# Kernel optimization log

Measured on AMD Instinct MI355X. Metric: run time of the kernel, lower is better.

Reference implementation:

```python
import jax, jax.numpy as jnp
import numpy as np

HIDDEN = 4096
N_HEADS = 32
N_KV_HEADS = 8
HEAD_DIM = HIDDEN // N_HEADS  # 128
N_REP = N_HEADS // N_KV_HEADS  # 4
ROPE_THETA = 10000.0
B, S = 2, 2048


def setup_inputs() -> dict:
    key = jax.random.key(0)
    ks = jax.random.split(key, 9)
    sc = 1.0 / np.sqrt(HIDDEN)
    query = jax.random.normal(ks[0], (B, S, HIDDEN), jnp.float32)
    key_t = jax.random.normal(ks[1], (B, S, HIDDEN), jnp.float32)
    value = jax.random.normal(ks[2], (B, S, HIDDEN), jnp.float32)
    position_ids = jnp.sort(jax.random.randint(ks[3], (B, S), 0, S), axis=-1)
    Wq = jax.random.normal(ks[4], (HIDDEN, N_HEADS * HEAD_DIM), jnp.float32) * sc
    Wk = jax.random.normal(ks[5], (HIDDEN, N_KV_HEADS * HEAD_DIM), jnp.float32) * sc
    Wv = jax.random.normal(ks[6], (HIDDEN, N_KV_HEADS * HEAD_DIM), jnp.float32) * sc
    Wo = jax.random.normal(ks[7], (N_HEADS * HEAD_DIM, HIDDEN), jnp.float32) * sc
    return {"query": query, "key": key_t, "value": value,
            "position_ids": position_ids,
            "Wq": Wq, "Wk": Wk, "Wv": Wv, "Wo": Wo}


def _rotate_half(x):
    x1, x2 = jnp.split(x, 2, axis=-1)
    return jnp.concatenate((-x2, x1), axis=-1)


def _rope_cos_sin(position_ids):
    # inv_freq: [head_dim/2]
    inv_freq = 1.0 / (ROPE_THETA ** (jnp.arange(0, HEAD_DIM, 2, dtype=jnp.float32) / HEAD_DIM))
    # freqs: [B, S, head_dim/2] via per-position lookup (equiv. to cache gather cos_cached[position_ids])
    freqs = position_ids[..., None].astype(jnp.float32) * inv_freq
    emb = jnp.concatenate((freqs, freqs), axis=-1)          # [B, S, head_dim]
    return jnp.cos(emb)[:, None, :, :], jnp.sin(emb)[:, None, :, :]  # [B,1,S,hd]


def reference(query, key, value, position_ids, Wq, Wk, Wv, Wo):
    nb, q_len, _ = query.shape
    # QKV projections (bias-free linear)
    q = jnp.einsum('bse,ef->bsf', query, Wq).reshape(nb, q_len, N_HEADS, HEAD_DIM).transpose(0, 2, 1, 3)
    k = jnp.einsum('bse,ef->bsf', key, Wk).reshape(nb, q_len, N_KV_HEADS, HEAD_DIM).transpose(0, 2, 1, 3)
    v = jnp.einsum('bse,ef->bsf', value, Wv).reshape(nb, q_len, N_KV_HEADS, HEAD_DIM).transpose(0, 2, 1, 3)
    # RoPE
    cos, sin = _rope_cos_sin(position_ids)
    q = q * cos + _rotate_half(q) * sin
    k = k * cos + _rotate_half(k) * sin
    # GQA repeat_kv: [B, kvH, S, d] -> [B, H, S, d]
    k = jnp.repeat(k, N_REP, axis=1)
    v = jnp.repeat(v, N_REP, axis=1)
    # scaled dot-product attention (flash-attn semantics, no padding mask)
    scale = 1.0 / jnp.sqrt(jnp.asarray(HEAD_DIM, q.dtype))
    scores = jnp.einsum('bhqd,bhkd->bhqk', q, k) * scale
    probs = jax.nn.softmax(scores, axis=-1)
    ctx = jnp.einsum('bhqk,bhkd->bhqd', probs, v)
    ctx = ctx.transpose(0, 2, 1, 3).reshape(nb, q_len, N_HEADS * HEAD_DIM)
    return jnp.einsum('bsf,fe->bse', ctx, Wo)
```

## Files before the change

kernel.cpp:

```cpp
#include <hip/hip_runtime.h>
#include <hip/hip_bf16.h>

typedef __attribute__((ext_vector_type(8))) short bf16x8;
typedef __attribute__((ext_vector_type(4))) float f32x4;
typedef __attribute__((ext_vector_type(16))) float f32x16;
typedef __attribute__((ext_vector_type(2))) unsigned uint2x;

#define AS1(p) ((const __attribute__((address_space(1))) void*)(p))
#define AS3(p) ((__attribute__((address_space(3))) void*)(p))

__device__ inline unsigned cvtpk_bf16(float lo, float hi) {
  unsigned r;
  asm("v_cvt_pk_bf16_f32 %0, %1, %2" : "=v"(r) : "v"(lo), "v"(hi));
  return r;
}

__device__ inline uint2x plswap(unsigned a, unsigned b) {
  return __builtin_amdgcn_permlane32_swap(a, b, false, false);
}


__global__ __launch_bounds__(256) void xconv_kv(const float* __restrict__ k_in,
                                                const float* __restrict__ v_in,
                                                __hip_bfloat16* __restrict__ kc,
                                                __hip_bfloat16* __restrict__ vc) {
  const float* in = blockIdx.y ? v_in : k_in;
  __hip_bfloat16* out = blockIdx.y ? vc : kc;
  size_t i = ((size_t)blockIdx.x * 256 + threadIdx.x) * 4;
  float4 v = *(const float4*)(in + i);
  union { __hip_bfloat16 h[4]; ushort4 u; } o;
  o.h[0] = __float2bfloat16(v.x);
  o.h[1] = __float2bfloat16(v.y);
  o.h[2] = __float2bfloat16(v.z);
  o.h[3] = __float2bfloat16(v.w);
  *(ushort4*)(out + i) = o.u;
}

__global__ __launch_bounds__(256) void xconv(const float* __restrict__ in,
                                             __hip_bfloat16* __restrict__ out) {
  size_t i = ((size_t)blockIdx.x * 256 + threadIdx.x) * 4;
  float4 v = *(const float4*)(in + i);
  union { __hip_bfloat16 h[4]; ushort4 u; } o;
  o.h[0] = __float2bfloat16(v.x);
  o.h[1] = __float2bfloat16(v.y);
  o.h[2] = __float2bfloat16(v.z);
  o.h[3] = __float2bfloat16(v.w);
  *(ushort4*)(out + i) = o.u;
}

__global__ __launch_bounds__(256) void wtransAll(const float* __restrict__ Wq,
                                                 const float* __restrict__ Wo,
                                                 const float* __restrict__ Wk,
                                                 const float* __restrict__ Wv,
                                                 __hip_bfloat16* __restrict__ WqT,
                                                 __hip_bfloat16* __restrict__ WoT,
                                                 __hip_bfloat16* __restrict__ WkT,
                                                 __hip_bfloat16* __restrict__ WvT) {
  const int z = blockIdx.z;
  const int N = (z < 2) ? 4096 : 1024;
  const int n0 = blockIdx.x << 6;
  if (n0 >= N) return;
  const float* W = (z == 0) ? Wq : (z == 1) ? Wo : (z == 2) ? Wk : Wv;
  __hip_bfloat16* WT = (z == 0) ? WqT : (z == 1) ? WoT : (z == 2) ? WkT : WvT;
  __shared__ float t[64][68];
  const int k0 = blockIdx.y << 6;
  const int tx = threadIdx.x & 15, ty = threadIdx.x >> 4;
#pragma unroll
  for (int j = 0; j < 4; ++j) {
    const int k = ty + j * 16;
    float4 v = *(const float4*)(W + (size_t)(k0 + k) * N + n0 + tx * 4);
    t[tx * 4 + 0][k] = v.x;
    t[tx * 4 + 1][k] = v.y;
    t[tx * 4 + 2][k] = v.z;
    t[tx * 4 + 3][k] = v.w;
  }
  __syncthreads();
#pragma unroll
  for (int j = 0; j < 4; ++j) {
    const int n = ty + j * 16;
    float4 v = *(const float4*)(&t[n][tx * 4]);
    union { __hip_bfloat16 h[4]; ushort4 u; } o;
    o.h[0] = __float2bfloat16(v.x);
    o.h[1] = __float2bfloat16(v.y);
    o.h[2] = __float2bfloat16(v.z);
    o.h[3] = __float2bfloat16(v.w);
    *(ushort4*)(WT + (size_t)(n0 + n) * 4096 + k0 + tx * 4) = o.u;
  }
}

__global__ __launch_bounds__(256) void rope(__hip_bfloat16* __restrict__ X,
                                            const int* __restrict__ pos,
                                            int hbits, float scale) {
  const int t = blockIdx.x * 256 + threadIdx.x;
  const int j = t & 63;
  const int rest = t >> 6;
  const int h = rest & ((1 << hbits) - 1);
  const int row = rest >> hbits;
  const float p = (float)pos[row];
  const float fr = p * exp2f((float)j * -0.2076205059304601f);
  float sn, cs;
  __sincosf(fr, &sn, &cs);
  const size_t base = (((size_t)row << hbits) + h) * 128 + j;
  const float x0 = __bfloat162float(X[base]);
  const float x1 = __bfloat162float(X[base + 64]);
  X[base]      = __float2bfloat16((x0 * cs - x1 * sn) * scale);
  X[base + 64] = __float2bfloat16((x1 * cs + x0 * sn) * scale);
}


__device__ inline int tile_off(int row, int k) {
  return (((row >> 4) << 1) + (k >> 5)) * 512 + (row & 15) * 32 +
         ((k & 31) ^ ((row & 8) << 1));
}

__device__ inline void stageA(const __hip_bfloat16* __restrict__ src, int ld, int row0,
                              int kt, int h, __hip_bfloat16* ldsT, int w, int lane) {
#pragma unroll
  for (int li = 0; li < 2; ++li) {
    const int t = li * 8 + w;
    const int grp = ((t >> 3) << 1) + h;
    const int srl = (t & 7) >> 1, sk = t & 1;
    const int rowbase = grp * 64 + srl * 16;
    __hip_bfloat16* dst = ldsT + ((((rowbase >> 4) << 1) + sk) << 9);
    const int r = lane >> 2;
    const int ku = (lane & 3) ^ ((r & 8) >> 2);
    __builtin_amdgcn_global_load_lds(
        AS1(src + (size_t)(row0 + rowbase + r) * ld + kt + (sk << 5) + (ku << 3)),
        AS3(dst), 16, 0, 0);
  }
}

__device__ inline void stageB(const __hip_bfloat16* __restrict__ src, int ld, int col0,
                              int kt, int h, __hip_bfloat16* ldsT, int w, int lane) {
#pragma unroll
  for (int li = 0; li < 2; ++li) {
    const int t = li * 8 + w;
    const int q = t >> 2;
    const int srl = (t >> 1) & 1, sk = t & 1;
    const int colbase = q * 64 + h * 32 + srl * 16;
    __hip_bfloat16* dst = ldsT + ((((colbase >> 4) << 1) + sk) << 9);
    const int r = lane >> 2;
    const int ku = (lane & 3) ^ ((r & 8) >> 2);
    __builtin_amdgcn_global_load_lds(
        AS1(src + (size_t)(col0 + colbase + r) * ld + kt + (sk << 5) + (ku << 3)),
        AS3(dst), 16, 0, 0);
  }
}

template <int OUT_F32>
__global__ __launch_bounds__(512, 1) void gemm256(const __hip_bfloat16* __restrict__ A,
                                                  const __hip_bfloat16* __restrict__ BT,
                                                  void* __restrict__ Cout,
                                                  int M, int N, int K) {
  __shared__ __align__(16) __hip_bfloat16 lds[2][2][16384];
  const int tid = threadIdx.x;
  const int lane = tid & 63, w = tid >> 6;
  const int l15 = lane & 15, lg = lane >> 4;
  const int wm = w >> 2, wn = w & 3;
  const int nbx = N >> 8;
  const int nwg = (M >> 8) * nbx;
  const int bid = blockIdx.x;
  const int swz = (bid & 7) * (nwg >> 3) + (bid >> 3);
  const int m0 = (swz / nbx) << 8, n0 = (swz % nbx) << 8;

  f32x4 acc[8][4] = {};
  const int NT = K >> 6;

  stageA(A, K, m0, 0, 0, &lds[0][0][0], w, lane);
  stageB(BT, K, n0, 0, 0, &lds[0][1][0], w, lane);
  stageA(A, K, m0, 0, 1, &lds[0][0][0], w, lane);
  stageB(BT, K, n0, 0, 1, &lds[0][1][0], w, lane);
  stageA(A, K, m0, 64, 0, &lds[1][0][0], w, lane);
  stageB(BT, K, n0, 64, 0, &lds[1][1][0], w, lane);
  asm volatile("s_waitcnt vmcnt(4)" ::: "memory");
  __builtin_amdgcn_s_barrier();

  for (int j = 0; j < NT; ++j) {
    const int buf = j & 1;
    const __hip_bfloat16* Ab = &lds[buf][0][0];
    const __hip_bfloat16* Bb = &lds[buf][1][0];
    __hip_bfloat16* An = &lds[buf ^ 1][0][0];
    __hip_bfloat16* Bn = &lds[buf ^ 1][1][0];
    __hip_bfloat16* Ac = &lds[buf][0][0];
    __hip_bfloat16* Bc = &lds[buf][1][0];
    const int kt1 = (j + 1) << 6, kt2 = (j + 2) << 6;
    const bool s1 = (j + 1) < NT, s2 = (j + 2) < NT;

    auto phase = [&](int rq, int cq, int sid) {
      bf16x8 af[2][4], bfr[2][2];
#pragma unroll
      for (int kk = 0; kk < 2; ++kk) {
#pragma unroll
        for (int rf = 0; rf < 4; ++rf)
          af[kk][rf] = *(const bf16x8*)(Ab +
              tile_off(wm * 128 + (rq * 4 + rf) * 16 + l15, kk * 32 + lg * 8));
#pragma unroll
        for (int cf = 0; cf < 2; ++cf)
          bfr[kk][cf] = *(const bf16x8*)(Bb +
              tile_off(wn * 64 + (cq * 2 + cf) * 16 + l15, kk * 32 + lg * 8));
      }
      if (sid == 0)      { if (s1) stageA(A, K, m0, kt1, 1, An, w, lane); }
      else if (sid == 1) { if (s1) stageB(BT, K, n0, kt1, 1, Bn, w, lane); }
      else if (sid == 2) { if (s2) stageA(A, K, m0, kt2, 0, Ac, w, lane); }
      else {
        if (s2) stageB(BT, K, n0, kt2, 0, Bc, w, lane);
        if (s2) asm volatile("s_waitcnt vmcnt(4)" ::: "memory");
        else    asm volatile("s_waitcnt vmcnt(0)" ::: "memory");
      }
      __builtin_amdgcn_s_barrier();
      asm volatile("s_waitcnt lgkmcnt(0)" ::: "memory");
      __builtin_amdgcn_sched_barrier(0);
      __builtin_amdgcn_s_setprio(1);
#pragma unroll
      for (int kk = 0; kk < 2; ++kk)
#pragma unroll
        for (int rf = 0; rf < 4; ++rf)
#pragma unroll
          for (int cf = 0; cf < 2; ++cf)
            acc[rq * 4 + rf][cq * 2 + cf] = __builtin_amdgcn_mfma_f32_16x16x32_bf16(
                af[kk][rf], bfr[kk][cf], acc[rq * 4 + rf][cq * 2 + cf], 0, 0, 0);
      __builtin_amdgcn_s_setprio(0);
      __builtin_amdgcn_s_barrier();
    };
    phase(0, 0, 0);
    phase(0, 1, 1);
    phase(1, 0, 2);
    phase(1, 1, 3);
  }

#pragma unroll
  for (int rf = 0; rf < 8; ++rf)
#pragma unroll
    for (int cf = 0; cf < 4; ++cf)
#pragma unroll
      for (int i = 0; i < 4; ++i) {
        const size_t row = (size_t)(m0 + wm * 128 + rf * 16 + lg * 4 + i);
        const size_t col = (size_t)(n0 + wn * 64 + cf * 16 + l15);
        if (OUT_F32)
          ((float*)Cout)[row * N + col] = acc[rf][cf][i];
        else
          ((__hip_bfloat16*)Cout)[row * N + col] = __float2bfloat16(acc[rf][cf][i]);
      }
}

__global__ __launch_bounds__(512, 1) void gemm_kv8(const __hip_bfloat16* __restrict__ Ak,
                                                   const __hip_bfloat16* __restrict__ Av,
                                                   const __hip_bfloat16* __restrict__ BkT,
                                                   const __hip_bfloat16* __restrict__ BvT,
                                                   __hip_bfloat16* __restrict__ Kp,
                                                   __hip_bfloat16* __restrict__ VT) {
  __shared__ __align__(16) __hip_bfloat16 lds[2][24576];
  const int zz = blockIdx.z;
  const __hip_bfloat16* A  = zz ? Av : Ak;
  const __hip_bfloat16* BT = zz ? BvT : BkT;
  const int K = 4096;
  const int tid = threadIdx.x;
  const int lane = tid & 63, w = tid >> 6;
  const int l15 = lane & 15, lg = lane >> 4;
  const int wm = w >> 2, wn = w & 3;
  const int bid = blockIdx.x;
  const int swz = (bid & 7) * 16 + (bid >> 3);
  const int m0 = (swz >> 2) << 7;
  const int n0 = (swz & 3) << 8;

  auto stgA = [&](int kt, int h, __hip_bfloat16* ldsA) {
    const int r16 = 2 * h + ((w >> 2) << 2) + ((w >> 1) & 1);
    const int sk = w & 1;
    __hip_bfloat16* dst = ldsA + (((r16 << 1) + sk) << 9);
    const int r = lane >> 2;
    const int ku = (lane & 3) ^ ((r & 8) >> 2);
    __builtin_amdgcn_global_load_lds(
        AS1(A + (size_t)(m0 + r16 * 16 + r) * K + kt + (sk << 5) + (ku << 3)),
        AS3(dst), 16, 0, 0);
  };
  auto stgB = [&](int kt, int h, __hip_bfloat16* ldsB) {
#pragma unroll
    for (int li = 0; li < 2; ++li) {
      const int idx = li * 8 + w;
      const int r16 = ((idx >> 2) << 2) + 2 * h + ((idx >> 1) & 1);
      const int sk = idx & 1;
      __hip_bfloat16* dst = ldsB + (((r16 << 1) + sk) << 9);
      const int r = lane >> 2;
      const int ku = (lane & 3) ^ ((r & 8) >> 2);
      __builtin_amdgcn_global_load_lds(
          AS1(BT + (size_t)(n0 + r16 * 16 + r) * K + kt + (sk << 5) + (ku << 3)),
          AS3(dst), 16, 0, 0);
    }
  };

  f32x4 acc[4][4] = {};
  const int NT = K >> 6;

  stgA(0, 0, &lds[0][0]);
  stgB(0, 0, &lds[0][8192]);
  stgA(0, 1, &lds[0][0]);
  stgB(0, 1, &lds[0][8192]);
  stgA(64, 0, &lds[1][0]);
  stgB(64, 0, &lds[1][8192]);
  asm volatile("s_waitcnt vmcnt(3)" ::: "memory");
  __builtin_amdgcn_s_barrier();

  for (int j = 0; j < NT; ++j) {
    const int buf = j & 1;
    const __hip_bfloat16* Ab = &lds[buf][0];
    const __hip_bfloat16* Bb = &lds[buf][8192];
    __hip_bfloat16* An = &lds[buf ^ 1][0];
    __hip_bfloat16* Bn = &lds[buf ^ 1][8192];
    __hip_bfloat16* Ac = &lds[buf][0];
    __hip_bfloat16* Bc = &lds[buf][8192];
    const int kt1 = (j + 1) << 6, kt2 = (j + 2) << 6;
    const bool s1 = (j + 1) < NT, s2 = (j + 2) < NT;

    auto phase = [&](int rq, int cq, int sid) {
      bf16x8 af[2][2], bfr[2][2];
#pragma unroll
      for (int kk = 0; kk < 2; ++kk) {
#pragma unroll
        for (int rf = 0; rf < 2; ++rf)
          af[kk][rf] = *(const bf16x8*)(Ab +
              tile_off(wm * 64 + (rq * 2 + rf) * 16 + l15, kk * 32 + lg * 8));
#pragma unroll
        for (int cf = 0; cf < 2; ++cf)
          bfr[kk][cf] = *(const bf16x8*)(Bb +
              tile_off(wn * 64 + (cq * 2 + cf) * 16 + l15, kk * 32 + lg * 8));
      }
      if (sid == 0)      { if (s1) stgA(kt1, 1, An); }
      else if (sid == 1) { if (s1) stgB(kt1, 1, Bn); }
      else if (sid == 2) { if (s2) stgA(kt2, 0, Ac); }
      else {
        if (s2) stgB(kt2, 0, Bc);
        if (s2) asm volatile("s_waitcnt vmcnt(3)" ::: "memory");
        else    asm volatile("s_waitcnt vmcnt(0)" ::: "memory");
      }
      __builtin_amdgcn_s_barrier();
      asm volatile("s_waitcnt lgkmcnt(0)" ::: "memory");
      __builtin_amdgcn_sched_barrier(0);
      __builtin_amdgcn_s_setprio(1);
#pragma unroll
      for (int kk = 0; kk < 2; ++kk)
#pragma unroll
        for (int rf = 0; rf < 2; ++rf)
#pragma unroll
          for (int cf = 0; cf < 2; ++cf)
            acc[rq * 2 + rf][cq * 2 + cf] = __builtin_amdgcn_mfma_f32_16x16x32_bf16(
                af[kk][rf], bfr[kk][cf], acc[rq * 2 + rf][cq * 2 + cf], 0, 0, 0);
      __builtin_amdgcn_s_setprio(0);
      __builtin_amdgcn_s_barrier();
    };
    phase(0, 0, 0);
    phase(0, 1, 1);
    phase(1, 0, 2);
    phase(1, 1, 3);
  }

  if (zz == 0) {
#pragma unroll
    for (int rf = 0; rf < 4; ++rf)
#pragma unroll
      for (int cf = 0; cf < 4; ++cf)
#pragma unroll
        for (int i = 0; i < 4; ++i) {
          const size_t row = (size_t)(m0 + wm * 64 + rf * 16 + lg * 4 + i);
          const size_t col = (size_t)(n0 + wn * 64 + cf * 16 + l15);
          Kp[row * 1024 + col] = __float2bfloat16(acc[rf][cf][i]);
        }
  } else {
    const int b = m0 >> 11, s0g = m0 & 2047;
#pragma unroll
    for (int rf = 0; rf < 4; ++rf)
#pragma unroll
      for (int cf = 0; cf < 4; ++cf) {
        const int d = n0 + wn * 64 + cf * 16 + l15;
        const int g = d >> 7, dl = d & 127;
        const int srow = s0g + wm * 64 + rf * 16 + lg * 4;
        union { __hip_bfloat16 h[4]; unsigned long long u; } pkv;
#pragma unroll
        for (int i = 0; i < 4; ++i) pkv.h[i] = __float2bfloat16(acc[rf][cf][i]);
        *(unsigned long long*)(VT + ((size_t)(b * 8 + g) * 128 + dl) * 2048 + srow) = pkv.u;
      }
  }
}

__global__ __launch_bounds__(512) void attn(const __hip_bfloat16* __restrict__ Q,
                                            const __hip_bfloat16* __restrict__ Kp,
                                            const __hip_bfloat16* __restrict__ VT,
                                            const int* __restrict__ pos,
                                            __hip_bfloat16* __restrict__ ctx,
                                            float qs) {
  const int tid = threadIdx.x;
  const int lane = tid & 63, w = tid >> 6;
  const int l31 = lane & 31, hi = lane >> 5;
  const int qt = blockIdx.x, h = blockIdx.y, b = blockIdx.z;
  const int kvh = h >> 2;
  const int q0 = qt * 256 + w * 32;

  const __hip_bfloat16* Qh = Q + (size_t)(b * 2048) * 4096 + h * 128;
  const __hip_bfloat16* Kh = Kp + (size_t)(b * 2048) * 1024 + kvh * 128;
  const __hip_bfloat16* Vh = VT + (size_t)(b * 8 + kvh) * 128 * 2048;

  __shared__ __hip_bfloat16 Ks[2][64 * 128];
  __shared__ __hip_bfloat16 Vs[2][128 * 64];

  auto stage = [&](int buf, int s0) {
#pragma unroll
    for (int j = 0; j < 2; ++j) {
      const int idx = w * 64 + lane + j * 512;
      const int rK = idx >> 4, uK = idx & 15;
      __builtin_amdgcn_global_load_lds(
          AS1(Kh + (size_t)(s0 + rK) * 1024 + ((uK ^ (rK & 7)) << 3)),
          AS3(&Ks[buf][(w * 64 + j * 512) * 8]), 16, 0, 0);
      const int rV = idx >> 3, uV = idx & 7;
      __builtin_amdgcn_global_load_lds(
          AS1(Vh + (size_t)rV * 2048 + s0 + ((uV ^ (rV & 7)) << 3)),
          AS3(&Vs[buf][(w * 64 + j * 512) * 8]), 16, 0, 0);
    }
  };

  stage(0, 0);

  const int qrow = q0 + l31;
  const float pp = (float)pos[b * 2048 + qrow];
  bf16x8 qf[8];
  {
#pragma unroll
    for (int kd = 0; kd < 4; ++kd) {
      bf16x8 rlo = *(const bf16x8*)(Qh + (size_t)qrow * 4096 + kd * 16 + hi * 8);
      bf16x8 rhi = *(const bf16x8*)(Qh + (size_t)qrow * 4096 + (kd + 4) * 16 + hi * 8);
      bf16x8 olo, ohi;
#pragma unroll
      for (int e = 0; e < 8; ++e) {
        const int j = kd * 16 + hi * 8 + e;
        const float fr = pp * exp2f((float)j * -0.2076205059304601f);
        float sn, cs;
        __sincosf(fr, &sn, &cs);
        const float x0 = __uint_as_float(((unsigned)(unsigned short)rlo[e]) << 16);
        const float x1 = __uint_as_float(((unsigned)(unsigned short)rhi[e]) << 16);
        __hip_bfloat16 h0 = __float2bfloat16((x0 * cs - x1 * sn) * qs);
        __hip_bfloat16 h1 = __float2bfloat16((x1 * cs + x0 * sn) * qs);
        olo[e] = *(short*)&h0;
        ohi[e] = *(short*)&h1;
      }
      qf[kd] = olo;
      qf[kd + 4] = ohi;
    }
  }

  f32x16 o[4] = {};
  float m = -1e30f, lsum = 0.f;
  __syncthreads();

  auto tile = [&](int tt, int cur, bool pf) {
    if (pf) stage(cur ^ 1, (tt + 1) * 64);

    f32x16 p[2] = {};
    __builtin_amdgcn_s_setprio(1);
#pragma unroll
    for (int n = 0; n < 2; ++n)
#pragma unroll
      for (int kd = 0; kd < 8; ++kd) {
        const int row = n * 32 + l31;
        bf16x8 kf = *(const bf16x8*)(&Ks[cur][row * 128 + (((2 * kd + hi) ^ (row & 7)) << 3)]);
        p[n] = __builtin_amdgcn_mfma_f32_32x32x16_bf16(kf, qf[kd], p[n], 0, 0, 0);
      }
    __builtin_amdgcn_s_setprio(0);

    float t16[16], t8[8], t4[4];
#pragma unroll
    for (int e = 0; e < 16; ++e) t16[e] = fmaxf(p[0][e], p[1][e]);
#pragma unroll
    for (int e = 0; e < 8; ++e) t8[e] = fmaxf(t16[e], t16[e + 8]);
#pragma unroll
    for (int e = 0; e < 4; ++e) t4[e] = fmaxf(t8[e], t8[e + 4]);
    float pmax = fmaxf(fmaxf(t4[0], t4[1]), fmaxf(t4[2], t4[3]));
    {
      uint2x r = plswap(__float_as_uint(pmax), __float_as_uint(pmax));
      pmax = fmaxf(__uint_as_float(r[0]), __uint_as_float(r[1]));
    }
    if (!__all(pmax - m <= 8.0f)) {
      const float mnew = fmaxf(m, pmax);
      const float fac = exp2f(m - mnew);
      m = mnew;
      lsum *= fac;
#pragma unroll
      for (int dc = 0; dc < 4; ++dc)
#pragma unroll
        for (int e = 0; e < 16; ++e) o[dc][e] *= fac;
    }
#pragma unroll
    for (int n = 0; n < 2; ++n)
#pragma unroll
      for (int e = 0; e < 16; ++e) p[n][e] = exp2f(p[n][e] - m);
    float s16[16];
#pragma unroll
    for (int e = 0; e < 16; ++e) s16[e] = p[0][e] + p[1][e];
#pragma unroll
    for (int e = 0; e < 8; ++e) s16[e] = s16[e] + s16[e + 8];
#pragma unroll
    for (int e = 0; e < 4; ++e) s16[e] = s16[e] + s16[e + 4];
    float rs = (s16[0] + s16[1]) + (s16[2] + s16[3]);
    {
      uint2x r = plswap(__float_as_uint(rs), __float_as_uint(rs));
      rs = __uint_as_float(r[0]) + __uint_as_float(r[1]);
    }
    lsum += rs;

    __builtin_amdgcn_s_setprio(1);
#pragma unroll
    for (int n = 0; n < 2; ++n)
#pragma unroll
      for (int ks = 0; ks < 2; ++ks) {
        const int bse = ks * 8;
        unsigned a1 = cvtpk_bf16(p[n][bse + 0], p[n][bse + 1]);
        unsigned b1 = cvtpk_bf16(p[n][bse + 4], p[n][bse + 5]);
        unsigned a2 = cvtpk_bf16(p[n][bse + 2], p[n][bse + 3]);
        unsigned b2 = cvtpk_bf16(p[n][bse + 6], p[n][bse + 7]);
        uint2x s1 = plswap(a1, b1);
        uint2x s2 = plswap(a2, b2);
        union { unsigned u[4]; bf16x8 v; } pw = {{s1[0], s2[0], s1[1], s2[1]}};
        const int slot = n * 2 + ks;
#pragma unroll
        for (int dc = 0; dc < 4; ++dc) {
          const int row = dc * 32 + l31;
          bf16x8 vf = *(const bf16x8*)(&Vs[cur][row * 64 + (((2 * slot + hi) ^ (row & 7)) << 3)]);
          o[dc] = __builtin_amdgcn_mfma_f32_32x32x16_bf16(vf, pw.v, o[dc], 0, 0, 0);
        }
      }
    __builtin_amdgcn_s_setprio(0);
    __syncthreads();
  };

  for (int t2 = 0; t2 < 16; ++t2) {
    tile(2 * t2, 0, true);
    tile(2 * t2 + 1, 1, t2 < 15);
  }

  const float inv = 1.0f / lsum;
  const size_t rowbase = ((size_t)(b * 2048 + q0 + l31)) * 4096 + h * 128;
#pragma unroll
  for (int dc = 0; dc < 4; ++dc)
#pragma unroll
    for (int g = 0; g < 4; ++g) {
      union { unsigned short us[4]; ushort4 u4; } pk;
#pragma unroll
      for (int e = 0; e < 4; ++e) {
        __hip_bfloat16 hv = __float2bfloat16(o[dc][g * 4 + e] * inv);
        pk.us[e] = *(unsigned short*)&hv;
      }
      *(ushort4*)(ctx + rowbase + dc * 32 + g * 8 + hi * 4) = pk.u4;
    }
}


extern "C" void kernel_launch(void* const* d_in, const int* in_sizes, int n_in,
                              void* d_out, int out_size, void* d_ws, size_t ws_size,
                              hipStream_t stream) {
  const float* q_in = (const float*)d_in[0];
  const float* k_in = (const float*)d_in[1];
  const float* v_in = (const float*)d_in[2];
  const int* pos    = (const int*)d_in[3];
  const float* Wq   = (const float*)d_in[4];
  const float* Wk   = (const float*)d_in[5];
  const float* Wv   = (const float*)d_in[6];
  const float* Wo   = (const float*)d_in[7];

  char* ws = (char*)d_ws;
  __hip_bfloat16* xbuf = (__hip_bfloat16*)(ws);
  __hip_bfloat16* WqT  = (__hip_bfloat16*)(ws + 33554432);
  __hip_bfloat16* WkT  = (__hip_bfloat16*)(ws + 67108864);
  __hip_bfloat16* WvT  = (__hip_bfloat16*)(ws + 75497472);
  __hip_bfloat16* WoT  = (__hip_bfloat16*)(ws + 83886080);
  __hip_bfloat16* Qp   = (__hip_bfloat16*)(ws + 117440512);
  __hip_bfloat16* Kp   = (__hip_bfloat16*)(ws + 150994944);
  __hip_bfloat16* VTb  = (__hip_bfloat16*)(ws + 167772160);
  __hip_bfloat16* vconv = WqT;

  wtransAll<<<dim3(64, 64, 4), 256, 0, stream>>>(Wq, Wo, Wk, Wv, WqT, WoT, WkT, WvT);
  xconv<<<16384, 256, 0, stream>>>(q_in, xbuf);
  gemm256<0><<<256, 512, 0, stream>>>(xbuf, WqT, Qp, 4096, 4096, 4096);
  xconv_kv<<<dim3(16384, 2), 256, 0, stream>>>(k_in, v_in, xbuf, vconv);
  gemm_kv8<<<dim3(128, 1, 2), 512, 0, stream>>>(xbuf, vconv, WkT, WvT, Kp, VTb);
  rope<<<8192, 256, 0, stream>>>(Kp, pos, 3, 1.0f);
  attn<<<dim3(8, 32, 2), 512, 0, stream>>>(Qp, Kp, VTb, pos, xbuf,
                                           0.08838834764831845f * 1.4426950408889634f);
  gemm256<1><<<256, 512, 0, stream>>>(xbuf, WoT, d_out, 4096, 4096, 4096);
}
```

Baseline: 627.1 us.

## Software-pipeline QK^T of next tile with softmax and PV of current tile

Splits K and V staging so K is prefetched two tiles ahead and V one tile ahead. The QK^T MFMAs for tile j+1 are issued in the same block as the PV MFMAs for tile j, after softmax, so the softmax's scalar and exp work can overlap with matrix-core work across waves. This costs extra registers for the next tile's scores and the packed probabilities, which may lower occupancy, and it makes the buffer indexing more intricate.

```diff
diff --git a/kernel.cpp b/kernel.cpp
--- a/kernel.cpp
+++ b/kernel.cpp
@@ -401,22 +401,30 @@
   __shared__ __hip_bfloat16 Ks[2][64 * 128];
   __shared__ __hip_bfloat16 Vs[2][128 * 64];
 
-  auto stage = [&](int buf, int s0) {
-#pragma unroll
-    for (int j = 0; j < 2; ++j) {
-      const int idx = w * 64 + lane + j * 512;
+  auto stageK = [&](int buf, int s0) {
+#pragma unroll
+    for (int jj = 0; jj < 2; ++jj) {
+      const int idx = w * 64 + lane + jj * 512;
       const int rK = idx >> 4, uK = idx & 15;
       __builtin_amdgcn_global_load_lds(
           AS1(Kh + (size_t)(s0 + rK) * 1024 + ((uK ^ (rK & 7)) << 3)),
-          AS3(&Ks[buf][(w * 64 + j * 512) * 8]), 16, 0, 0);
+          AS3(&Ks[buf][(w * 64 + jj * 512) * 8]), 16, 0, 0);
+    }
+  };
+  auto stageV = [&](int buf, int s0) {
+#pragma unroll
+    for (int jj = 0; jj < 2; ++jj) {
+      const int idx = w * 64 + lane + jj * 512;
       const int rV = idx >> 3, uV = idx & 7;
       __builtin_amdgcn_global_load_lds(
           AS1(Vh + (size_t)rV * 2048 + s0 + ((uV ^ (rV & 7)) << 3)),
-          AS3(&Vs[buf][(w * 64 + j * 512) * 8]), 16, 0, 0);
+          AS3(&Vs[buf][(w * 64 + jj * 512) * 8]), 16, 0, 0);
     }
   };
 
-  stage(0, 0);
+  stageK(0, 0);
+  stageV(0, 0);
+  stageK(1, 64);
 
   const int qrow = q0 + l31;
   const float pp = (float)pos[b * 2048 + qrow];
@@ -446,23 +454,32 @@
   }
 
   f32x16 o[4] = {};
+  f32x16 p[2];
   float m = -1e30f, lsum = 0.f;
   __syncthreads();
 
-  auto tile = [&](int tt, int cur, bool pf) {
-    if (pf) stage(cur ^ 1, (tt + 1) * 64);
-
-    f32x16 p[2] = {};
+  {
     __builtin_amdgcn_s_setprio(1);
 #pragma unroll
-    for (int n = 0; n < 2; ++n)
+    for (int n = 0; n < 2; ++n) {
+      f32x16 a = {};
 #pragma unroll
       for (int kd = 0; kd < 8; ++kd) {
         const int row = n * 32 + l31;
-        bf16x8 kf = *(const bf16x8*)(&Ks[cur][row * 128 + (((2 * kd + hi) ^ (row & 7)) << 3)]);
-        p[n] = __builtin_amdgcn_mfma_f32_32x32x16_bf16(kf, qf[kd], p[n], 0, 0, 0);
-      }
+        bf16x8 kf = *(const bf16x8*)(&Ks[0][row * 128 + (((2 * kd + hi) ^ (row & 7)) << 3)]);
+        a = __builtin_amdgcn_mfma_f32_32x32x16_bf16(kf, qf[kd], a, 0, 0, 0);
+      }
+      p[n] = a;
+    }
     __builtin_amdgcn_s_setprio(0);
+  }
+  __syncthreads();
+
+  auto tile = [&](int j, int cur) {
+    const bool sK = (j + 2) < 32;
+    const bool sV = (j + 1) < 32;
+    if (sK) stageK(cur, (j + 2) * 64);
+    if (sV) stageV(cur ^ 1, (j + 1) * 64);
 
     float t16[16], t8[8], t4[4];
 #pragma unroll
@@ -504,7 +521,7 @@
     }
     lsum += rs;
 
-    __builtin_amdgcn_s_setprio(1);
+    bf16x8 paf[4];
 #pragma unroll
     for (int n = 0; n < 2; ++n)
 #pragma unroll
@@ -517,21 +534,38 @@
         uint2x s1 = plswap(a1, b1);
         uint2x s2 = plswap(a2, b2);
         union { unsigned u[4]; bf16x8 v; } pw = {{s1[0], s2[0], s1[1], s2[1]}};
-        const int slot = n * 2 + ks;
-#pragma unroll
-        for (int dc = 0; dc < 4; ++dc) {
-          const int row = dc * 32 + l31;
-          bf16x8 vf = *(const bf16x8*)(&Vs[cur][row * 64 + (((2 * slot + hi) ^ (row & 7)) << 3)]);
-          o[dc] = __builtin_amdgcn_mfma_f32_32x32x16_bf16(vf, pw.v, o[dc], 0, 0, 0);
+        paf[n * 2 + ks] = pw.v;
+      }
+
+    __builtin_amdgcn_s_setprio(1);
+    if (sV) {
+#pragma unroll
+      for (int n = 0; n < 2; ++n) {
+        f32x16 a = {};
+#pragma unroll
+        for (int kd = 0; kd < 8; ++kd) {
+          const int row = n * 32 + l31;
+          bf16x8 kf = *(const bf16x8*)(&Ks[cur ^ 1][row * 128 + (((2 * kd + hi) ^ (row & 7)) << 3)]);
+          a = __builtin_amdgcn_mfma_f32_32x32x16_bf16(kf, qf[kd], a, 0, 0, 0);
         }
+        p[n] = a;
+      }
+    }
+#pragma unroll
+    for (int slot = 0; slot < 4; ++slot)
+#pragma unroll
+      for (int dc = 0; dc < 4; ++dc) {
+        const int row = dc * 32 + l31;
+        bf16x8 vf = *(const bf16x8*)(&Vs[cur][row * 64 + (((2 * slot + hi) ^ (row & 7)) << 3)]);
+        o[dc] = __builtin_amdgcn_mfma_f32_32x32x16_bf16(vf, paf[slot], o[dc], 0, 0, 0);
       }
     __builtin_amdgcn_s_setprio(0);
     __syncthreads();
   };
 
   for (int t2 = 0; t2 < 16; ++t2) {
-    tile(2 * t2, 0, true);
-    tile(2 * t2 + 1, 1, t2 < 15);
+    tile(2 * t2, 0);
+    tile(2 * t2 + 1, 1);
   }
 
   const float inv = 1.0f / lsum;
```

Measured after the change: 628.1 us. About the same (+0.2%).
